# Kernel tuning notes

Hardware: AMD Instinct MI355X
Metric: run time of the kernel (lower is better)

The kernel has to match this reference:

```python
import jax, jax.numpy as jnp
import numpy as np
from jax import lax

# Config constants (Mamba2 mixer)
HIDDEN = 2048
EXPAND = 2
INTER = EXPAND * HIDDEN          # 4096
NHEADS = 64
HEADDIM = 64                     # INTER == NHEADS * HEADDIM
DSTATE = 128
NGROUPS = 1
KCONV = 4
CHUNK = 256
CONV_DIM = INTER + 2 * NGROUPS * DSTATE   # 4352
PROJ = INTER + CONV_DIM + NHEADS          # 8512
EPS = 1e-6
BATCH, SEQ = 2, 2048


def setup_inputs() -> dict:
    key = jax.random.key(0)
    ks = jax.random.split(key, 8)
    return {
        "hidden_states": jax.random.normal(ks[0], (BATCH, SEQ, HIDDEN), jnp.float32),
        "in_proj_w": jax.random.normal(ks[1], (PROJ, HIDDEN), jnp.float32) * 0.02,
        "conv_w": jax.random.normal(ks[2], (CONV_DIM, 1, KCONV), jnp.float32) * 0.2,
        "conv_b": jax.random.normal(ks[3], (CONV_DIM,), jnp.float32) * 0.02,
        "dt_bias": jnp.ones((NHEADS,), jnp.float32),
        "A_log": jnp.log(jnp.arange(1, NHEADS + 1, dtype=jnp.float32)),
        "D": jnp.ones((NHEADS,), jnp.float32),
        "norm_weight": jnp.ones((INTER,), jnp.float32),
        "out_proj_w": jax.random.normal(ks[4], (HIDDEN, INTER), jnp.float32) * 0.02,
    }


def _segsum(a):
    # a: [b,h,c,l] -> [b,h,c,l,l]; segsum[i,j] = sum_{j<k<=i} a[k], -inf above diag
    L = a.shape[-1]
    cs = jnp.cumsum(a, axis=-1)
    d = cs[..., :, None] - cs[..., None, :]
    mask = jnp.tril(jnp.ones((L, L), bool))
    return jnp.where(mask, d, -jnp.inf)


def reference(hidden_states, in_proj_w, conv_w, conv_b, dt_bias, A_log, D,
              norm_weight, out_proj_w):
    b, s, _ = hidden_states.shape
    # in_proj and split
    proj = hidden_states @ in_proj_w.T                       # [b,s,PROJ]
    gate = proj[..., :INTER]
    hbc = proj[..., INTER:INTER + CONV_DIM]
    dt = proj[..., INTER + CONV_DIM:]                        # [b,s,H]
    # depthwise causal conv1d + silu
    xc = jnp.swapaxes(hbc, 1, 2)                             # [b,CONV_DIM,s]
    conv = lax.conv_general_dilated(
        xc, conv_w, window_strides=(1,), padding=[(KCONV - 1, 0)],
        dimension_numbers=("NCH", "OIH", "NCH"), feature_group_count=CONV_DIM)
    conv = jax.nn.silu(conv + conv_b[None, :, None])
    hbc = jnp.swapaxes(conv, 1, 2)                           # [b,s,CONV_DIM]
    x = hbc[..., :INTER].reshape(b, s, NHEADS, HEADDIM)
    Bg = hbc[..., INTER:INTER + NGROUPS * DSTATE].reshape(b, s, NGROUPS, DSTATE)
    Cg = hbc[..., INTER + NGROUPS * DSTATE:].reshape(b, s, NGROUPS, DSTATE)
    # repeat_interleave groups -> heads
    Bh = jnp.repeat(Bg, NHEADS // NGROUPS, axis=2)           # [b,s,H,N]
    Ch = jnp.repeat(Cg, NHEADS // NGROUPS, axis=2)
    # dt and per-token decay
    dt = jax.nn.softplus(dt + dt_bias)                       # [b,s,H], dt_limit=(0,inf)
    A = -jnp.exp(A_log)                                      # [H]
    a = dt * A                                               # [b,s,H]
    # chunk views
    nc, L = s // CHUNK, CHUNK
    x_ = x.reshape(b, nc, L, NHEADS, HEADDIM)
    B_ = Bh.reshape(b, nc, L, NHEADS, DSTATE)
    C_ = Ch.reshape(b, nc, L, NHEADS, DSTATE)
    dt_ = dt.reshape(b, nc, L, NHEADS)
    a_ = jnp.transpose(a.reshape(b, nc, L, NHEADS), (0, 3, 1, 2))  # [b,H,c,l]
    cs = jnp.cumsum(a_, axis=-1)                             # [b,H,c,l]
    Lmat = jnp.exp(_segsum(a_))                              # [b,H,c,l,l]
    xdt = x_ * dt_[..., None]                                # [b,c,l,H,P]
    # intra-chunk (diagonal blocks)
    Y_diag = jnp.einsum("bclhn,bcshn,bhcls,bcshp->bclhp", C_, B_, Lmat, xdt)
    # per-chunk states
    decay_states = jnp.exp(cs[..., -1:] - cs)                # [b,H,c,l]
    states = jnp.einsum("bclhn,bhcl,bclhp->bchpn", B_, decay_states, xdt)
    chunk_decay = jnp.exp(cs[..., -1])                       # [b,H,c]
    # inter-chunk recurrence over chunks
    def step(carry, inp):
        dec, st = inp                                        # dec [b,H], st [b,H,P,N]
        return carry * dec[:, :, None, None] + st, carry
    init = jnp.zeros((b, NHEADS, HEADDIM, DSTATE), states.dtype)
    _, prev = lax.scan(step, init,
                       (jnp.moveaxis(chunk_decay, 2, 0), jnp.moveaxis(states, 1, 0)))
    prev = jnp.moveaxis(prev, 0, 1)                          # [b,c,H,P,N] state before chunk
    Y_off = jnp.einsum("bclhn,bchpn,bhcl->bclhp", C_, prev, jnp.exp(cs))
    y = (Y_diag + Y_off).reshape(b, s, NHEADS, HEADDIM) + x * D[None, None, :, None]
    y = y.reshape(b, s, INTER)
    # gated RMSNorm
    h = y.astype(jnp.float32) * jax.nn.silu(gate.astype(jnp.float32))
    var = jnp.mean(h * h, axis=-1, keepdims=True)
    h = norm_weight * (h * lax.rsqrt(var + EPS))
    # out_proj
    return h @ out_proj_w.T
```

## Files before the change

kernel.cpp:

```cpp
#include <hip/hip_runtime.h>

#define DEV __device__ __forceinline__

typedef unsigned short u16;
typedef unsigned int u32;
typedef __attribute__((ext_vector_type(4))) float f32x4;
typedef __attribute__((ext_vector_type(8))) u16 u16x8;
typedef __attribute__((ext_vector_type(4))) u16 u16x4;
typedef __attribute__((ext_vector_type(8))) __bf16 bf16x8;

#define INTER 4096
#define DSTATE 128
#define CONVD 4352
#define NPAD 8704
#define NROWS 4096

DEV float b2f(u16 u){ union{u32 i; float f;} v; v.i = ((u32)u)<<16; return v.f; }
DEV u16 f2b(float f){ union{u32 i; float f;} v; v.f = f; u32 r = v.i + 0x7fffu + ((v.i>>16)&1u); return (u16)(r>>16); }

typedef const __attribute__((address_space(1))) u32 gas_u32;
typedef __attribute__((address_space(3))) u32 las_u32;
DEV void gl_lds16(const u16* g, u16* l){
  __builtin_amdgcn_global_load_lds((gas_u32*)g, (las_u32*)l, 16, 0, 0);
}

__global__ __launch_bounds__(256) void k_cvt3(
    const float* __restrict__ X, const float* __restrict__ W1, const float* __restrict__ W2,
    u16* __restrict__ Xb, u16* __restrict__ Wb, u16* __restrict__ W2b)
{
  long b = blockIdx.x;
  const float* src; u16* dst; long n, base;
  if (b < 8192)       { src = X;  dst = Xb;  n = 8388608L;  base = b*1024L; }
  else if (b < 25600) { src = W1; dst = Wb;  n = 17432576L; base = (b-8192)*1024L; }
  else                { src = W2; dst = W2b; n = 8388608L;  base = (b-25600)*1024L; }
  long i = base + (long)threadIdx.x*4;
  u16x4 o;
  if (i < n){
    f32x4 v = *(const f32x4*)&src[i];
    o[0]=f2b(v[0]); o[1]=f2b(v[1]); o[2]=f2b(v[2]); o[3]=f2b(v[3]);
  } else {
    o[0]=0; o[1]=0; o[2]=0; o[3]=0;
  }
  *(u16x4*)&dst[i] = o;
}

template<int EPI>
__global__ __launch_bounds__(512, 2) void k_gemm8(
    const u16* __restrict__ A, const u16* __restrict__ B,
    void* __restrict__ C0, float* __restrict__ C1,
    int lda, int ldb, int ldc, int K, int NTM, long sCz)
{
  __shared__ __align__(16) char smem[131072];
  const int t = threadIdx.x, lane = t & 63, w = t >> 6;
  const int wm = w >> 2, wn = w & 3, w64 = w * 64;
  const int NT = K >> 6, NIT = NT >> 1;
  const int z = blockIdx.y;

  const int nwg = gridDim.x;
  const int orig = blockIdx.x;
  const int wg = (orig & 7) * (nwg >> 3) + (orig >> 3);
  const int mt = wg % NTM, nt = wg / NTM;

  const u16* Ab = A + (long)mt * 256 * lda + (long)z * K;
  const u16* Bb = B + (long)nt * 256 * ldb + (long)z * K;

  const int laneoff = (lane & 15) * 64 + (lane >> 4) * 16;
  const int lo = laneoff ^ (((laneoff >> 9) & 1) << 5);

  long aoff[2], boff[2];
#pragma unroll
  for (int q = 0; q < 2; q++) {
    int u = t + q * 512;
    int up = u ^ (((u >> 5) & 1) << 1);
    int row = (up >> 6) * 16 + ((up & 63) >> 2);
    int c8 = (up & 3) * 8;
    aoff[q] = (long)row * lda + c8;
    boff[q] = (long)row * ldb + c8;
  }

  f32x4 acc[8][4];
#pragma unroll
  for (int i=0;i<8;i++)
#pragma unroll
    for (int j=0;j<4;j++) acc[i][j] = (f32x4){0.f,0.f,0.f,0.f};

#define SA(BUF,KH,KT) do{ long kb_ = (long)(KT)*64 + (KH)*32; \
    gl_lds16(Ab + aoff[0] + kb_, (u16*)(smem + (BUF)*65536 + (KH)*16384 + w64*16)); \
    gl_lds16(Ab + aoff[1] + kb_, (u16*)(smem + (BUF)*65536 + (KH)*16384 + 8192 + w64*16)); }while(0)
#define SB(BUF,KH,KT) do{ long kb_ = (long)(KT)*64 + (KH)*32; \
    gl_lds16(Bb + boff[0] + kb_, (u16*)(smem + (BUF)*65536 + 32768 + (KH)*16384 + w64*16)); \
    gl_lds16(Bb + boff[1] + kb_, (u16*)(smem + (BUF)*65536 + 32768 + (KH)*16384 + 8192 + w64*16)); }while(0)

#define SPHASE(BUF,KH,STMT,VM,HASV) do{ \
    const char* pa_ = smem + (BUF)*65536 + (KH)*16384; \
    const char* pb_ = smem + (BUF)*65536 + 32768 + (KH)*16384; \
    STMT; \
    bf16x8 a_[8], b_[4]; \
    _Pragma("unroll") \
    for (int j_=0;j_<4;j_++) b_[j_] = *(const bf16x8*)(pb_ + (wn*4+j_)*1024 + lo); \
    _Pragma("unroll") \
    for (int m_=0;m_<8;m_++) a_[m_] = *(const bf16x8*)(pa_ + (wm*8+m_)*1024 + lo); \
    __builtin_amdgcn_s_setprio(1); \
    _Pragma("unroll") \
    for (int m_=0;m_<8;m_++) \
      _Pragma("unroll") \
      for (int j_=0;j_<4;j_++) \
        acc[m_][j_] = __builtin_amdgcn_mfma_f32_16x16x32_bf16(a_[m_], b_[j_], acc[m_][j_], 0,0,0); \
    __builtin_amdgcn_s_setprio(0); \
     \
    __builtin_amdgcn_sched_group_barrier(0x100, 6, 0); \
    if (HASV) __builtin_amdgcn_sched_group_barrier(0x010, 4, 0); \
    _Pragma("unroll") \
    for (int g_=0; g_<6; ++g_){ \
      __builtin_amdgcn_sched_group_barrier(0x008, 4, 0); \
      __builtin_amdgcn_sched_group_barrier(0x100, 1, 0); \
    } \
    __builtin_amdgcn_sched_group_barrier(0x008, 8, 0); \
    if ((VM)==1) asm volatile("s_waitcnt vmcnt(8)":::"memory"); \
    if ((VM)==2) asm volatile("s_waitcnt vmcnt(4)":::"memory"); \
    if ((VM)==3) asm volatile("s_waitcnt vmcnt(0)":::"memory"); \
    asm volatile("s_barrier":::"memory"); \
  }while(0)

  SA(0,0,0); SB(0,0,0); SA(0,1,0); SB(0,1,0); SA(1,0,1); SB(1,0,1);
  asm volatile("s_waitcnt vmcnt(8)":::"memory");
  asm volatile("s_barrier":::"memory");

  for (int it = 0; it < NIT-1; ++it) {
    int t1 = 2*it+1, t2 = 2*it+2, t3 = 2*it+3;
    SPHASE(0,0, { SA(1,1,t1); SB(1,1,t1); }, 1, 1);
    SPHASE(0,1, { SA(0,0,t2); SB(0,0,t2); }, 1, 1);
    SPHASE(1,0, { SA(0,1,t2); SB(0,1,t2); }, 1, 1);
    SPHASE(1,1, { SA(1,0,t3); SB(1,0,t3); }, 1, 1);
  }
  {
    int tl = NT-1;
    SPHASE(0,0, { SA(1,1,tl); SB(1,1,tl); }, 1, 1);
    SPHASE(0,1, ((void)0), 2, 0);
    SPHASE(1,0, ((void)0), 3, 0);
    SPHASE(1,1, ((void)0), 0, 0);
  }
#undef SA
#undef SB
#undef SPHASE

#pragma unroll
  for (int i=0;i<8;i++)
#pragma unroll
    for (int j=0;j<4;j++)
#pragma unroll
      for (int r=0;r<4;r++){
        int gm = mt*256 + wm*128 + i*16 + (lane>>4)*4 + r;
        int gn = nt*256 + wn*64 + j*16 + (lane&15);
        float v = acc[i][j][r];
        if (EPI==0){
          ((u16*)C0)[(long)gm*ldc + gn] = f2b(v);
          if (gn >= 8448 && gn < 8512) C1[(long)gm*64 + (gn-8448)] = v;
        } else {
          ((float*)C0)[(long)z*sCz + (long)gm*ldc + gn] = v;
        }
      }
}

__global__ __launch_bounds__(256) void k_add(const float* __restrict__ p, float* __restrict__ out, long n){
  long i = ((long)blockIdx.x*256 + threadIdx.x)*8;
  if (i >= n) return;
  f32x4 a0 = *(const f32x4*)&p[i];
  f32x4 a1 = *(const f32x4*)&p[i+4];
  f32x4 b0 = *(const f32x4*)&p[n+i];
  f32x4 b1 = *(const f32x4*)&p[n+i+4];
  a0 += b0; a1 += b1;
  *(f32x4*)&out[i] = a0;
  *(f32x4*)&out[i+4] = a1;
}

template<int EPI>
__global__ __launch_bounds__(256) void k_gemm_bt(
    const u16* __restrict__ A, const u16* __restrict__ B,
    void* __restrict__ C0, float* __restrict__ C1,
    int lda, int ldb, int ldc, int K,
    long sAz, long sBz, long sCz, int auxcol)
{
  __shared__ u16 As[128*64];
  __shared__ u16 Bs[128*64];
  const int t = threadIdx.x, w = t>>6, lane = t&63;
  const int mt = blockIdx.y, nt = blockIdx.x, z = blockIdx.z;
  const u16* Ab = A + (long)z*sAz + (long)mt*128*lda;
  const u16* Bb = B + (long)z*sBz + (long)nt*128*ldb;
  const int wm = w>>1, wn = w&1;
  f32x4 acc[4][4];
#pragma unroll
  for (int i=0;i<4;i++)
#pragma unroll
    for (int j=0;j<4;j++) acc[i][j] = (f32x4){0.f,0.f,0.f,0.f};
  const int srow = (lane>>3), scol = (lane&7)*8;
  for (int k0=0; k0<K; k0+=64){
#pragma unroll
    for (int i=0;i<4;i++){
      int ch = w*4+i;
      int row = ch*8 + srow;
      gl_lds16(Ab + (long)row*lda + k0 + scol, As + ch*512);
      gl_lds16(Bb + (long)row*ldb + k0 + scol, Bs + ch*512);
    }
    __syncthreads();
#pragma unroll
    for (int kk=0;kk<2;kk++){
      bf16x8 af[4], bfr[4];
#pragma unroll
      for (int i=0;i<4;i++) af[i]  = *(const bf16x8*)&As[(wm*64+i*16+(lane&15))*64 + kk*32 + (lane>>4)*8];
#pragma unroll
      for (int j=0;j<4;j++) bfr[j] = *(const bf16x8*)&Bs[(wn*64+j*16+(lane&15))*64 + kk*32 + (lane>>4)*8];
#pragma unroll
      for (int i=0;i<4;i++)
#pragma unroll
        for (int j=0;j<4;j++)
          acc[i][j] = __builtin_amdgcn_mfma_f32_16x16x32_bf16(af[i], bfr[j], acc[i][j], 0,0,0);
    }
    __syncthreads();
  }
#pragma unroll
  for (int i=0;i<4;i++)
#pragma unroll
    for (int j=0;j<4;j++)
#pragma unroll
      for (int r=0;r<4;r++){
        int gm = mt*128 + wm*64 + i*16 + (lane>>4)*4 + r;
        int gn = nt*128 + wn*64 + j*16 + (lane&15);
        float v = acc[i][j][r];
        if (EPI==0){
          ((u16*)C0)[(long)gm*ldc + gn] = f2b(v);
          if (gn >= auxcol) C1[(long)gm*128 + (gn-auxcol)] = v;
        } else {
          ((float*)C0)[(long)z*sCz + (long)gm*ldc + gn] = v;
        }
      }
}

__global__ __launch_bounds__(256) void k_conv(
    const u16* __restrict__ Pb, const float* __restrict__ cw, const float* __restrict__ cb,
    u16* __restrict__ XBC)
{
  long tg = (long)blockIdx.x*256 + threadIdx.x;
  int row = (int)(tg/544);
  int ch0 = (int)(tg%544)*8;
  int s = row & 2047;
  float acc[8];
#pragma unroll
  for (int j=0;j<8;j++) acc[j] = cb[ch0+j];
#pragma unroll
  for (int k=0;k<4;k++){
    int sk = s - 3 + k;
    if (sk >= 0){
      u16x8 v = *(const u16x8*)&Pb[(long)(row-3+k)*NPAD + INTER + ch0];
#pragma unroll
      for (int j=0;j<8;j++) acc[j] += b2f(v[j]) * cw[(ch0+j)*4 + k];
    }
  }
  u16x8 o;
#pragma unroll
  for (int j=0;j<8;j++){ float x = acc[j]; o[j] = f2b(x/(1.f+__expf(-x))); }
  *(u16x8*)&XBC[(long)row*CONVD + ch0] = o;
}

__global__ __launch_bounds__(256) void k_dtcs(
    const float* __restrict__ DTraw, const float* __restrict__ dt_bias,
    const float* __restrict__ A_log,
    float* __restrict__ dtb, float* __restrict__ csb, float* __restrict__ cdec)
{
  __shared__ float sc[256];
  int bid = blockIdx.x;
  int bh = bid>>3, c = bid&7;
  int h = bh & 63, b = bh>>6;
  int l = threadIdx.x;
  int row = (b*8+c)*256 + l;
  float x = DTraw[(long)row*64 + h] + dt_bias[h];
  float dt = (x > 20.f) ? x : log1pf(__expf(x));
  float a = dt * (-__expf(A_log[h]));
  dtb[(long)row*64 + h] = dt;
  sc[l] = a; __syncthreads();
  for (int off=1; off<256; off<<=1){
    float v = (l>=off) ? sc[l-off] : 0.f;
    __syncthreads();
    sc[l] += v;
    __syncthreads();
  }
  float cs = sc[l];
  csb[(long)bid*256 + l] = cs;
  if (l==255) cdec[bid] = __expf(cs);
}

__global__ __launch_bounds__(256) void k_states(
    const u16* __restrict__ XBC, const float* __restrict__ dtb, const float* __restrict__ csb,
    float* __restrict__ states)
{
  __shared__ u16 xsT[64*136];
  __shared__ u16 bsT[128*136];
  __shared__ float dtl[128], del[128];
  int bid = blockIdx.x;
  int h = bid & 63, bc = bid >> 6;
  int b = bc>>3, c = bc&7;
  int rowb = bc*256;
  int t = threadIdx.x, w = t>>6, lane = t&63;
  int csbase = ((b*64+h)*8 + c)*256;
  float clast = csb[csbase + 255];
  f32x4 acc[8];
#pragma unroll
  for (int j=0;j<8;j++) acc[j] = (f32x4){0.f,0.f,0.f,0.f};
  for (int half=0; half<2; half++){
    int lbase = half*128;
    if (t < 128){
      dtl[t] = dtb[(long)(rowb+lbase+t)*64 + h];
      del[t] = __expf(clast - csb[csbase + lbase + t]);
    }
    __syncthreads();
#pragma unroll
    for (int it=0; it<4; it++){
      int id = it*256+t;
      int p8 = id&7, l = id>>3;
      u16x8 v = *(const u16x8*)&XBC[(long)(rowb+lbase+l)*CONVD + h*64 + p8*8];
      float d = dtl[l];
#pragma unroll
      for (int j=0;j<8;j++) xsT[(p8*8+j)*136 + l] = f2b(b2f(v[j])*d);
    }
#pragma unroll
    for (int it=0; it<8; it++){
      int id = it*256+t;
      int n8 = id&15, l = id>>4;
      u16x8 v = *(const u16x8*)&XBC[(long)(rowb+lbase+l)*CONVD + INTER + n8*8];
      float d = del[l];
#pragma unroll
      for (int j=0;j<8;j++) bsT[(n8*8+j)*136 + l] = f2b(b2f(v[j])*d);
    }
    __syncthreads();
#pragma unroll
    for (int ks=0; ks<4; ks++){
      bf16x8 af = *(const bf16x8*)&xsT[(w*16 + (lane&15))*136 + ks*32 + (lane>>4)*8];
#pragma unroll
      for (int j=0;j<8;j++){
        bf16x8 bf = *(const bf16x8*)&bsT[(j*16 + (lane&15))*136 + ks*32 + (lane>>4)*8];
        acc[j] = __builtin_amdgcn_mfma_f32_16x16x32_bf16(af, bf, acc[j], 0,0,0);
      }
    }
    __syncthreads();
  }
  float* outp = states + (long)bid*8192;
#pragma unroll
  for (int j=0;j<8;j++)
#pragma unroll
    for (int r=0;r<4;r++){
      int gm = w*16 + (lane>>4)*4 + r;
      int gn = j*16 + (lane&15);
      outp[gm*128 + gn] = acc[j][r];
    }
}

__global__ __launch_bounds__(256) void k_scan(
    const float* __restrict__ states, const float* __restrict__ cdec,
    u16* __restrict__ prevb)
{
  int bid = blockIdx.x;
  int bh = bid>>3, sub = bid&7;
  int b = bh>>6, h = bh&63;
  int e = (sub*256 + threadIdx.x)*4;
  f32x4 carry = (f32x4){0.f,0.f,0.f,0.f};
#pragma unroll
  for (int c=0;c<8;c++){
    long idx = ((long)((b*8+c)*64 + h))*8192 + e;
    u16x4 o;
    o[0]=f2b(carry[0]); o[1]=f2b(carry[1]); o[2]=f2b(carry[2]); o[3]=f2b(carry[3]);
    *(u16x4*)&prevb[idx] = o;
    f32x4 s = *(const f32x4*)&states[idx];
    float d = cdec[bh*8 + c];
    carry = carry*d + s;
  }
}

__global__ __launch_bounds__(256) void k_ydiag(
    const u16* __restrict__ XBC, const float* __restrict__ G,
    const u16* __restrict__ prevb, const float* __restrict__ dtb,
    const float* __restrict__ csb, const float* __restrict__ Dp,
    float* __restrict__ Y)
{
  __shared__ u16 PA[256*72];
  __shared__ u16 PB[64*72];
  __shared__ float csl[256];
  int bid = blockIdx.x;
  int h = bid&63, bc = bid>>6;
  int b = bc>>3, c = bc&7;
  int rowb = bc*256;
  int t = threadIdx.x, w = t>>6, lane = t&63;
  int csbase = ((b*64+h)*8 + c)*256;
  csl[t] = csb[csbase + t];
  const float* Gz = G + (long)bc*65536;
  f32x4 ad[4][4], ao[4][4];
#pragma unroll
  for (int i=0;i<4;i++)
#pragma unroll
    for (int j=0;j<4;j++){ ad[i][j]=(f32x4){0.f,0.f,0.f,0.f}; ao[i][j]=(f32x4){0.f,0.f,0.f,0.f}; }
  __syncthreads();
  for (int sl6=0; sl6<6; sl6++){
    if (sl6 < 4){
      int s0 = sl6*64;
#pragma unroll
      for (int r=0;r<8;r++){
        int id = r*256+t;
        int l = id>>3, sc8 = (id&7)*8;
        f32x4 g0 = *(const f32x4*)&Gz[l*256 + s0+sc8];
        f32x4 g1 = *(const f32x4*)&Gz[l*256 + s0+sc8+4];
        float cl = csl[l];
        u16x8 o;
#pragma unroll
        for (int jj=0;jj<4;jj++){
          int s = s0+sc8+jj;
          o[jj] = (s<=l) ? f2b(g0[jj]*__expf(cl - csl[s])) : (u16)0;
        }
#pragma unroll
        for (int jj=4;jj<8;jj++){
          int s = s0+sc8+jj;
          o[jj] = (s<=l) ? f2b(g1[jj-4]*__expf(cl - csl[s])) : (u16)0;
        }
        *(u16x8*)&PA[l*72 + sc8] = o;
      }
#pragma unroll
      for (int r=0;r<16;r++){
        int id = r*256+t;
        int p = id&63, ks = id>>6;
        float xv = b2f(XBC[(long)(rowb+s0+ks)*CONVD + h*64 + p]);
        float d = dtb[(long)(rowb+s0+ks)*64 + h];
        PB[p*72 + ks] = f2b(xv*d);
      }
    } else {
      int n0 = (sl6-4)*64;
#pragma unroll
      for (int r=0;r<8;r++){
        int id = r*256+t;
        int l = id>>3, kc = (id&7)*8;
        u16x8 v = *(const u16x8*)&XBC[(long)(rowb+l)*CONVD + INTER + DSTATE + n0 + kc];
        *(u16x8*)&PA[l*72 + kc] = v;
      }
#pragma unroll
      for (int r=0;r<2;r++){
        int id = r*256+t;
        int p = id>>3, kc = (id&7)*8;
        u16x8 v = *(const u16x8*)&prevb[((long)bid*64 + p)*128 + n0 + kc];
        *(u16x8*)&PB[p*72 + kc] = v;
      }
    }
    __syncthreads();
#pragma unroll
    for (int kk=0;kk<2;kk++){
      bf16x8 af[4], bfr[4];
#pragma unroll
      for (int i=0;i<4;i++) af[i]  = *(const bf16x8*)&PA[(w*64+i*16+(lane&15))*72 + kk*32 + (lane>>4)*8];
#pragma unroll
      for (int j=0;j<4;j++) bfr[j] = *(const bf16x8*)&PB[(j*16+(lane&15))*72 + kk*32 + (lane>>4)*8];
      if (sl6 < 4){
#pragma unroll
        for (int i=0;i<4;i++)
#pragma unroll
          for (int j=0;j<4;j++)
            ad[i][j] = __builtin_amdgcn_mfma_f32_16x16x32_bf16(af[i], bfr[j], ad[i][j], 0,0,0);
      } else {
#pragma unroll
        for (int i=0;i<4;i++)
#pragma unroll
          for (int j=0;j<4;j++)
            ao[i][j] = __builtin_amdgcn_mfma_f32_16x16x32_bf16(af[i], bfr[j], ao[i][j], 0,0,0);
      }
    }
    __syncthreads();
  }
  float Dh = Dp[h];
#pragma unroll
  for (int i=0;i<4;i++)
#pragma unroll
    for (int j=0;j<4;j++)
#pragma unroll
      for (int r=0;r<4;r++){
        int l = w*64 + i*16 + (lane>>4)*4 + r;
        int p = j*16 + (lane&15);
        float e = __expf(csl[l]);
        float xv = b2f(XBC[(long)(rowb+l)*CONVD + h*64 + p]);
        float v = ad[i][j][r] + e*ao[i][j][r] + Dh*xv;
        Y[(long)(rowb+l)*INTER + h*64 + p] = v;
      }
}

__global__ __launch_bounds__(256) void k_norm(
    const float* __restrict__ Y, const u16* __restrict__ Pb,
    const float* __restrict__ nw, u16* __restrict__ hb)
{
  int row = blockIdx.x, t = threadIdx.x;
  int w = t>>6, lane = t&63;
  float hv[16];
  float ss = 0.f;
#pragma unroll
  for (int r=0;r<4;r++){
    int idx = (r*256+t)*4;
    f32x4 yv = *(const f32x4*)&Y[(long)row*INTER + idx];
    u16x4 gv = *(const u16x4*)&Pb[(long)row*NPAD + idx];
#pragma unroll
    for (int jj=0;jj<4;jj++){
      float g = b2f(gv[jj]);
      float hh = yv[jj] * g / (1.f+__expf(-g));
      hv[r*4+jj] = hh;
      ss += hh*hh;
    }
  }
  for (int off=32; off; off>>=1) ss += __shfl_down(ss, off);
  __shared__ float sm[4];
  if (lane==0) sm[w]=ss;
  __syncthreads();
  float tot = sm[0]+sm[1]+sm[2]+sm[3];
  float sc = rsqrtf(tot/4096.f + 1e-6f);
#pragma unroll
  for (int r=0;r<4;r++){
    int idx = (r*256+t)*4;
    f32x4 nv = *(const f32x4*)&nw[idx];
    u16x4 o;
#pragma unroll
    for (int jj=0;jj<4;jj++) o[jj] = f2b(hv[r*4+jj]*nv[jj]*sc);
    *(u16x4*)&hb[(long)row*INTER + idx] = o;
  }
}

extern "C" void kernel_launch(void* const* d_in, const int* in_sizes, int n_in,
                              void* d_out, int out_size, void* d_ws, size_t ws_size,
                              hipStream_t stream)
{
  (void)in_sizes; (void)n_in;
  const float* X    = (const float*)d_in[0];
  const float* W1   = (const float*)d_in[1];
  const float* CW   = (const float*)d_in[2];
  const float* CB   = (const float*)d_in[3];
  const float* DTB  = (const float*)d_in[4];
  const float* ALOG = (const float*)d_in[5];
  const float* DD   = (const float*)d_in[6];
  const float* NW   = (const float*)d_in[7];
  const float* W2   = (const float*)d_in[8];
  float* out = (float*)d_out;
  char* ws = (char*)d_ws;

  constexpr long OFF_XB    = 0L;
  constexpr long OFF_WB    = 16777216L;
  constexpr long OFF_Y     = 0L;
  constexpr long OFF_P01   = 0L;
  constexpr long OFF_ST    = 67108864L;
  constexpr long OFF_HB    = 67108864L;
  constexpr long OFF_W2B   = 100663296L;
  constexpr long OFF_PB    = 117440512L;
  constexpr long OFF_DTRAW = 188743680L;
  constexpr long OFF_XBC   = 189792256L;
  constexpr long OFF_DT    = 225443840L;
  constexpr long OFF_CS    = 226492416L;
  constexpr long OFF_CDEC  = 227540992L;
  constexpr long OFF_G     = 227545088L;
  constexpr long OFF_PREV  = 231739392L;
  constexpr long WS_NEEDED = 248516608L;

  if ((long)ws_size < WS_NEEDED){
    hipMemsetAsync(d_out, 0, (size_t)out_size*4, stream);
    return;
  }

  u16*   Xb    = (u16*)(ws + OFF_XB);
  u16*   Wb    = (u16*)(ws + OFF_WB);
  u16*   W2b   = (u16*)(ws + OFF_W2B);
  u16*   Pb    = (u16*)(ws + OFF_PB);
  float* DTraw = (float*)(ws + OFF_DTRAW);
  u16*   XBCb  = (u16*)(ws + OFF_XBC);
  float* dtb   = (float*)(ws + OFF_DT);
  float* csb   = (float*)(ws + OFF_CS);
  float* cdec  = (float*)(ws + OFF_CDEC);
  float* G     = (float*)(ws + OFF_G);
  float* st    = (float*)(ws + OFF_ST);
  u16*   prevb = (u16*)(ws + OFF_PREV);
  float* Y     = (float*)(ws + OFF_Y);
  float* P01   = (float*)(ws + OFF_P01);
  u16*   hb    = (u16*)(ws + OFF_HB);

  k_cvt3<<<33792, 256, 0, stream>>>(X, W1, W2, Xb, Wb, W2b);

  k_gemm8<0><<<dim3(544,1), 512, 0, stream>>>(Xb, Wb, Pb, DTraw, 2048, 2048, NPAD, 2048, 16, 0L);

  k_conv<<<8704, 256, 0, stream>>>(Pb, CW, CB, XBCb);

  k_dtcs<<<1024, 256, 0, stream>>>(DTraw, DTB, ALOG, dtb, csb, cdec);

  k_gemm_bt<1><<<dim3(2,2,16), 256, 0, stream>>>(XBCb + INTER + DSTATE, XBCb + INTER, G, nullptr,
      CONVD, CONVD, 256, 128, 256L*CONVD, 256L*CONVD, 65536L, 0);

  k_states<<<1024, 256, 0, stream>>>(XBCb, dtb, csb, st);

  k_scan<<<1024, 256, 0, stream>>>(st, cdec, prevb);

  k_ydiag<<<1024, 256, 0, stream>>>(XBCb, G, prevb, dtb, csb, DD, Y);

  k_norm<<<4096, 256, 0, stream>>>(Y, Pb, NW, hb);

  k_gemm8<1><<<dim3(128,2), 512, 0, stream>>>(hb, W2b, P01, nullptr, 4096, 4096, 2048, 2048, 16, 8388608L);
  k_add<<<8192, 256, 0, stream>>>(P01, out, 8388608L);
}
```

Baseline: 609.0 us.

## Add quadrant-phased bf16 GEMM kernel for in_proj with finer load/compute interleave

Adds a new GEMM kernel that splits each 64-wide K step into four quadrant phases, each covering half the rows and half the columns. Every phase issues one small global-to-LDS prefetch and runs 16 MFMAs, so loads are spread more evenly across compute. The in_proj GEMM is switched to this kernel. Each phase now ends in two barriers and an lgkmcnt(0) wait, which adds synchronisation overhead and may reduce overlap compared with the scheduler-group-barrier version.

```diff
diff --git a/kernel.cpp b/kernel.cpp
--- a/kernel.cpp
+++ b/kernel.cpp
@@ -42,6 +42,122 @@
     o[0]=0; o[1]=0; o[2]=0; o[3]=0;
   }
   *(u16x4*)&dst[i] = o;
+}
+
+template<int EPI>
+__global__ __launch_bounds__(512, 2) void k_gemmq(
+    const u16* __restrict__ A, const u16* __restrict__ B,
+    void* __restrict__ C0, float* __restrict__ C1,
+    int lda, int ldb, int ldc, int K, int NTM, long sCz)
+{
+  __shared__ __align__(16) char smem[131072];
+  const int t = threadIdx.x, lane = t & 63, w = t >> 6;
+  const int wm = w >> 2, wn = w & 3, w64 = w * 64;
+  const int NT = K >> 6;
+  const int z = blockIdx.y;
+
+  const int nwg = gridDim.x;
+  const int orig = blockIdx.x;
+  const int wg = (orig & 7) * (nwg >> 3) + (orig >> 3);
+  const int mt = wg % NTM, nt = wg / NTM;
+
+  const u16* Ab = A + (long)mt * 256 * lda + (long)z * K;
+  const u16* Bb = B + (long)nt * 256 * ldb + (long)z * K;
+
+  const int laneoff = (lane & 15) * 64 + (lane >> 4) * 16;
+  const int lo = laneoff ^ (((laneoff >> 9) & 1) << 5);
+
+  const int up = t ^ (((t >> 5) & 1) << 1);
+  const int srow = (up >> 6) * 16 + ((up & 63) >> 2);
+  const int sc8 = (up & 3) * 8;
+  const long aoff = (long)srow * lda + sc8;
+  const long boff = (long)srow * ldb + sc8;
+
+  f32x4 acc[8][4];
+#pragma unroll
+  for (int i=0;i<8;i++)
+#pragma unroll
+    for (int j=0;j<4;j++) acc[i][j] = (f32x4){0.f,0.f,0.f,0.f};
+
+  bf16x8 a_[4][2], b_[2][2];
+
+#define SAH(BUF,RH,KT) do{ \
+    gl_lds16(Ab + aoff + (long)(RH)*128*lda + (long)(KT)*64,      (u16*)(smem + (BUF)*65536 +         (RH)*8192 + w64*16)); \
+    gl_lds16(Ab + aoff + (long)(RH)*128*lda + (long)(KT)*64 + 32, (u16*)(smem + (BUF)*65536 + 16384 + (RH)*8192 + w64*16)); }while(0)
+#define SBH(BUF,RH,KT) do{ \
+    gl_lds16(Bb + boff + (long)(RH)*128*ldb + (long)(KT)*64,      (u16*)(smem + (BUF)*65536 + 32768 +         (RH)*8192 + w64*16)); \
+    gl_lds16(Bb + boff + (long)(RH)*128*ldb + (long)(KT)*64 + 32, (u16*)(smem + (BUF)*65536 + 32768 + 16384 + (RH)*8192 + w64*16)); }while(0)
+
+#define PH(BUF,RH,CH,RA,STMT,VM) do{ \
+    const char* pa_ = smem + (BUF)*65536; \
+    const char* pb_ = pa_ + 32768; \
+    if (RA){ \
+      _Pragma("unroll") for (int i_=0;i_<4;i_++) \
+        _Pragma("unroll") for (int k_=0;k_<2;k_++) \
+          a_[i_][k_] = *(const bf16x8*)(pa_ + k_*16384 + (wm*8+(RH)*4+i_)*1024 + lo); \
+    } \
+    _Pragma("unroll") for (int j_=0;j_<2;j_++) \
+      _Pragma("unroll") for (int k_=0;k_<2;k_++) \
+        b_[j_][k_] = *(const bf16x8*)(pb_ + k_*16384 + (wn*4+(CH)*2+j_)*1024 + lo); \
+    STMT; \
+    asm volatile("s_barrier":::"memory"); \
+    asm volatile("s_waitcnt lgkmcnt(0)":::"memory"); \
+    __builtin_amdgcn_sched_barrier(0); \
+    __builtin_amdgcn_s_setprio(1); \
+    _Pragma("unroll") for (int i_=0;i_<4;i_++) \
+      _Pragma("unroll") for (int j_=0;j_<2;j_++) \
+        _Pragma("unroll") for (int k_=0;k_<2;k_++) \
+          acc[(RH)*4+i_][(CH)*2+j_] = __builtin_amdgcn_mfma_f32_16x16x32_bf16(a_[i_][k_], b_[j_][k_], acc[(RH)*4+i_][(CH)*2+j_], 0,0,0); \
+    __builtin_amdgcn_s_setprio(0); \
+    if ((VM)==1) asm volatile("s_waitcnt vmcnt(2)":::"memory"); \
+    if ((VM)==2) asm volatile("s_waitcnt vmcnt(0)":::"memory"); \
+    asm volatile("s_barrier":::"memory"); \
+  }while(0)
+
+  SAH(0,0,0); SAH(0,1,0); SBH(0,0,0); SBH(0,1,0); SAH(1,0,1);
+  asm volatile("s_waitcnt vmcnt(2)":::"memory");
+  asm volatile("s_barrier":::"memory");
+
+  for (int u = 0; u <= NT-4; u += 2){
+    PH(0,0,0,1, SAH(1,1,u+1), 0);
+    PH(0,0,1,0, SBH(1,0,u+1), 0);
+    PH(0,1,0,1, SBH(1,1,u+1), 0);
+    PH(0,1,1,0, SAH(0,0,u+2), 1);
+    PH(1,0,0,1, SAH(0,1,u+2), 0);
+    PH(1,0,1,0, SBH(0,0,u+2), 0);
+    PH(1,1,0,1, SBH(0,1,u+2), 0);
+    PH(1,1,1,0, SAH(1,0,u+3), 1);
+  }
+  {
+    PH(0,0,0,1, SAH(1,1,NT-1), 0);
+    PH(0,0,1,0, SBH(1,0,NT-1), 0);
+    PH(0,1,0,1, SBH(1,1,NT-1), 0);
+    PH(0,1,1,0, ((void)0), 2);
+    PH(1,0,0,1, ((void)0), 0);
+    PH(1,0,1,0, ((void)0), 0);
+    PH(1,1,0,1, ((void)0), 0);
+    PH(1,1,1,0, ((void)0), 0);
+  }
+#undef SAH
+#undef SBH
+#undef PH
+
+#pragma unroll
+  for (int i=0;i<8;i++)
+#pragma unroll
+    for (int j=0;j<4;j++)
+#pragma unroll
+      for (int r=0;r<4;r++){
+        int gm = mt*256 + wm*128 + i*16 + (lane>>4)*4 + r;
+        int gn = nt*256 + wn*64 + j*16 + (lane&15);
+        float v = acc[i][j][r];
+        if (EPI==0){
+          ((u16*)C0)[(long)gm*ldc + gn] = f2b(v);
+          if (gn >= 8448 && gn < 8512) C1[(long)gm*64 + (gn-8448)] = v;
+        } else {
+          ((float*)C0)[(long)z*sCz + (long)gm*ldc + gn] = v;
+        }
+      }
 }
 
 template<int EPI>
@@ -107,7 +223,6 @@
       for (int j_=0;j_<4;j_++) \
         acc[m_][j_] = __builtin_amdgcn_mfma_f32_16x16x32_bf16(a_[m_], b_[j_], acc[m_][j_], 0,0,0); \
     __builtin_amdgcn_s_setprio(0); \
-     \
     __builtin_amdgcn_sched_group_barrier(0x100, 6, 0); \
     if (HASV) __builtin_amdgcn_sched_group_barrier(0x010, 4, 0); \
     _Pragma("unroll") \
@@ -581,7 +696,7 @@
 
   k_cvt3<<<33792, 256, 0, stream>>>(X, W1, W2, Xb, Wb, W2b);
 
-  k_gemm8<0><<<dim3(544,1), 512, 0, stream>>>(Xb, Wb, Pb, DTraw, 2048, 2048, NPAD, 2048, 16, 0L);
+  k_gemmq<0><<<dim3(544,1), 512, 0, stream>>>(Xb, Wb, Pb, DTraw, 2048, 2048, NPAD, 2048, 16, 0L);
 
   k_conv<<<8704, 256, 0, stream>>>(Pb, CW, CB, XBCb);
 
```

Measured after the change: 611.1 us. About the same (+0.3%).

## Replace split-K out_proj GEMM and add kernel with 256x128-tile full-K GEMM

Applied to the files above, without the earlier changes.

The out_proj GEMM previously used split-K with two partial fp32 outputs followed by a separate add kernel. It is replaced by a new 256x128-tile kernel that runs the full K=4096 reduction and writes straight to the output. The new kernel launches 256 workgroups with an XCD-aware tile remap, double-buffered LDS loads, and setprio around the MFMA blocks. This removes one launch and the partial-sum write and reread traffic, at the cost of fewer independent tiles and a longer serial K loop per workgroup.

```diff
diff --git a/kernel.cpp b/kernel.cpp
--- a/kernel.cpp
+++ b/kernel.cpp
@@ -162,16 +162,109 @@
       }
 }
 
-__global__ __launch_bounds__(256) void k_add(const float* __restrict__ p, float* __restrict__ out, long n){
-  long i = ((long)blockIdx.x*256 + threadIdx.x)*8;
-  if (i >= n) return;
-  f32x4 a0 = *(const f32x4*)&p[i];
-  f32x4 a1 = *(const f32x4*)&p[i+4];
-  f32x4 b0 = *(const f32x4*)&p[n+i];
-  f32x4 b1 = *(const f32x4*)&p[n+i+4];
-  a0 += b0; a1 += b1;
-  *(f32x4*)&out[i] = a0;
-  *(f32x4*)&out[i+4] = a1;
+__global__ __launch_bounds__(512, 2) void k_gemmN(
+    const u16* __restrict__ A, const u16* __restrict__ B, float* __restrict__ C0,
+    int lda, int ldb, int ldc, int K, int NTM)
+{
+  __shared__ __align__(16) char smem[98304];
+  const int t = threadIdx.x, lane = t & 63, w = t >> 6;
+  const int wm = w >> 2, wn = w & 3, w64 = w * 64;
+  const int NT = K >> 6, NIT = NT >> 1;
+
+  const int nwg = gridDim.x;
+  const int orig = blockIdx.x;
+  const int wg = (orig & 7) * (nwg >> 3) + (orig >> 3);
+  const int mt = wg % NTM, nt = wg / NTM;
+
+  const u16* Ab = A + (long)mt * 256 * lda;
+  const u16* Bb = B + (long)nt * 128 * ldb;
+
+  const int laneoff = (lane & 15) * 64 + (lane >> 4) * 16;
+  const int lo = laneoff ^ (((laneoff >> 9) & 1) << 5);
+
+  long aoff[2];
+#pragma unroll
+  for (int q = 0; q < 2; q++) {
+    int u = t + q * 512;
+    int up = u ^ (((u >> 5) & 1) << 1);
+    int row = (up >> 6) * 16 + ((up & 63) >> 2);
+    int c8 = (up & 3) * 8;
+    aoff[q] = (long)row * lda + c8;
+  }
+  long boff;
+  {
+    int up = t ^ (((t >> 5) & 1) << 1);
+    int row = (up >> 6) * 16 + ((up & 63) >> 2);
+    int c8 = (up & 3) * 8;
+    boff = (long)row * ldb + c8;
+  }
+
+  f32x4 acc[8][2];
+#pragma unroll
+  for (int i=0;i<8;i++)
+#pragma unroll
+    for (int j=0;j<2;j++) acc[i][j] = (f32x4){0.f,0.f,0.f,0.f};
+
+#define SAN(BUF,KH,KT) do{ long kb_ = (long)(KT)*64 + (KH)*32; \
+    gl_lds16(Ab + aoff[0] + kb_, (u16*)(smem + (BUF)*49152 + (KH)*16384 + w64*16)); \
+    gl_lds16(Ab + aoff[1] + kb_, (u16*)(smem + (BUF)*49152 + (KH)*16384 + 8192 + w64*16)); }while(0)
+#define SBN(BUF,KH,KT) do{ long kb_ = (long)(KT)*64 + (KH)*32; \
+    gl_lds16(Bb + boff + kb_, (u16*)(smem + (BUF)*49152 + 32768 + (KH)*8192 + w64*16)); }while(0)
+
+#define NPHASE(BUF,KH,STMT,VM) do{ \
+    const char* pa_ = smem + (BUF)*49152 + (KH)*16384; \
+    const char* pb_ = smem + (BUF)*49152 + 32768 + (KH)*8192; \
+    STMT; \
+    bf16x8 a_[8], b_[2]; \
+    _Pragma("unroll") \
+    for (int j_=0;j_<2;j_++) b_[j_] = *(const bf16x8*)(pb_ + (wn*2+j_)*1024 + lo); \
+    _Pragma("unroll") \
+    for (int m_=0;m_<8;m_++) a_[m_] = *(const bf16x8*)(pa_ + (wm*8+m_)*1024 + lo); \
+    __builtin_amdgcn_s_setprio(1); \
+    _Pragma("unroll") \
+    for (int m_=0;m_<8;m_++) \
+      _Pragma("unroll") \
+      for (int j_=0;j_<2;j_++) \
+        acc[m_][j_] = __builtin_amdgcn_mfma_f32_16x16x32_bf16(a_[m_], b_[j_], acc[m_][j_], 0,0,0); \
+    __builtin_amdgcn_s_setprio(0); \
+    if ((VM)==1) asm volatile("s_waitcnt vmcnt(6)":::"memory"); \
+    if ((VM)==2) asm volatile("s_waitcnt vmcnt(3)":::"memory"); \
+    if ((VM)==3) asm volatile("s_waitcnt vmcnt(0)":::"memory"); \
+    asm volatile("s_barrier":::"memory"); \
+  }while(0)
+
+  SAN(0,0,0); SBN(0,0,0); SAN(0,1,0); SBN(0,1,0); SAN(1,0,1); SBN(1,0,1);
+  asm volatile("s_waitcnt vmcnt(6)":::"memory");
+  asm volatile("s_barrier":::"memory");
+
+  for (int it = 0; it < NIT-1; ++it) {
+    int t1 = 2*it+1, t2 = 2*it+2, t3 = 2*it+3;
+    NPHASE(0,0, { SAN(1,1,t1); SBN(1,1,t1); }, 1);
+    NPHASE(0,1, { SAN(0,0,t2); SBN(0,0,t2); }, 1);
+    NPHASE(1,0, { SAN(0,1,t2); SBN(0,1,t2); }, 1);
+    NPHASE(1,1, { SAN(1,0,t3); SBN(1,0,t3); }, 1);
+  }
+  {
+    int tl = NT-1;
+    NPHASE(0,0, { SAN(1,1,tl); SBN(1,1,tl); }, 1);
+    NPHASE(0,1, ((void)0), 2);
+    NPHASE(1,0, ((void)0), 3);
+    NPHASE(1,1, ((void)0), 0);
+  }
+#undef SAN
+#undef SBN
+#undef NPHASE
+
+#pragma unroll
+  for (int i=0;i<8;i++)
+#pragma unroll
+    for (int j=0;j<2;j++)
+#pragma unroll
+      for (int r=0;r<4;r++){
+        int gm = mt*256 + wm*128 + i*16 + (lane>>4)*4 + r;
+        int gn = nt*128 + wn*32 + j*16 + (lane&15);
+        C0[(long)gm*ldc + gn] = acc[i][j][r];
+      }
 }
 
 template<int EPI>
@@ -544,7 +637,6 @@
   constexpr long OFF_XB    = 0L;
   constexpr long OFF_WB    = 16777216L;
   constexpr long OFF_Y     = 0L;
-  constexpr long OFF_P01   = 0L;
   constexpr long OFF_ST    = 67108864L;
   constexpr long OFF_HB    = 67108864L;
   constexpr long OFF_W2B   = 100663296L;
@@ -576,7 +668,6 @@
   float* st    = (float*)(ws + OFF_ST);
   u16*   prevb = (u16*)(ws + OFF_PREV);
   float* Y     = (float*)(ws + OFF_Y);
-  float* P01   = (float*)(ws + OFF_P01);
   u16*   hb    = (u16*)(ws + OFF_HB);
 
   k_cvt3<<<33792, 256, 0, stream>>>(X, W1, W2, Xb, Wb, W2b);
@@ -598,6 +689,5 @@
 
   k_norm<<<4096, 256, 0, stream>>>(Y, Pb, NW, hb);
 
-  k_gemm8<1><<<dim3(128,2), 512, 0, stream>>>(hb, W2b, P01, nullptr, 4096, 4096, 2048, 2048, 16, 8388608L);
-  k_add<<<8192, 256, 0, stream>>>(P01, out, 8388608L);
-}
+  k_gemmN<<<256, 512, 0, stream>>>(hb, W2b, out, 4096, 4096, 2048, 4096, 16);
+}
```

After: 595.4 us. 1.02x faster.
